# Performance work log

Hardware: AMD Instinct MI355X
Metric: run time of the kernel (lower is better)

## Reference

```python
import jax, jax.numpy as jnp
import numpy as np

D, H, E, K, S = 1024, 2048, 8, 2, 1  # dim, expert hidden, n_experts, top_k, n_shared
B, L = 4, 2048


def setup_inputs() -> dict:
    key = jax.random.key(0)
    ks = jax.random.split(key, 9)
    std = 0.02
    return {
        "x": jax.random.normal(ks[0], (B, L, D), dtype=jnp.float32),
        "router_w": jax.random.normal(ks[1], (E, D), dtype=jnp.float32) * std,
        "experts_bias": jnp.zeros((E,), dtype=jnp.float32),  # aux-free LB bias buffer
        "w1": jax.random.normal(ks[2], (E, D, H), dtype=jnp.float32) * std,
        "w3": jax.random.normal(ks[3], (E, D, H), dtype=jnp.float32) * std,
        "w2": jax.random.normal(ks[4], (E, H, D), dtype=jnp.float32) * std,
        "sw1": jax.random.normal(ks[5], (S, D, H), dtype=jnp.float32) * std,
        "sw3": jax.random.normal(ks[6], (S, D, H), dtype=jnp.float32) * std,
        "sw2": jax.random.normal(ks[7], (S, H, D), dtype=jnp.float32) * std,
    }


def reference(x, router_w, experts_bias, w1, w3, w2, sw1, sw3, sw2):
    b, l, d = x.shape
    xf = x.reshape(-1, d)  # [T, D], T = b*l

    # shared experts (SwiGLU FFN), summed over S
    sg = jnp.einsum("td,sdh->tsh", xf, sw1)
    su = jnp.einsum("td,sdh->tsh", xf, sw3)
    shared_out = jnp.einsum("tsh,shd->td", jax.nn.silu(sg) * su, sw2)

    # router + aux-free load-balancing bias
    logits = xf @ router_w.T + experts_bias  # [T, E]
    rw, sel = jax.lax.top_k(logits, K)       # [T, K]
    rw = jax.nn.softmax(rw.astype(jnp.float32), axis=-1).astype(x.dtype)

    # combine weights scattered to [T, E]; equals torch one_hot dispatch+index_add
    cw = (jax.nn.one_hot(sel, E, dtype=x.dtype) * rw[..., None]).sum(axis=1)

    # all-expert SwiGLU, weighted-combined (identical math: unselected weight = 0)
    g = jnp.einsum("td,edh->teh", xf, w1)
    u = jnp.einsum("td,edh->teh", xf, w3)
    eo = jax.nn.silu(g) * u  # [T, E, H]
    moe_out = jnp.einsum("te,teh,ehd->td", cw, eo, w2)

    return (moe_out + shared_out).reshape(b, l, d)
```

## Files before the change

### kernel.cpp

```cpp
#include <hip/hip_runtime.h>
#include <stdint.h>

#define T_TOK 8192
#define DIMV  1024
#define HIDV  2048
#define NE    8
#define CAP   8192
#define ASSIGN_TOT 24576

typedef __attribute__((ext_vector_type(8))) short          bf16x8;
typedef __attribute__((ext_vector_type(8))) unsigned short u16x8;
typedef __attribute__((ext_vector_type(4))) float          floatx4;

__device__ __forceinline__ unsigned short f2bf(float f) {
    union { float f; unsigned int i; } v; v.f = f;
    unsigned int i = v.i;
    return (unsigned short)((i + 0x7FFFu + ((i >> 16) & 1u)) >> 16);
}

__device__ __forceinline__ void gll16(const void* g, void* l) {
    __builtin_amdgcn_global_load_lds((const __attribute__((address_space(1))) void*)g,
                                     (__attribute__((address_space(3))) void*)l,
                                     16, 0, 0);
}

__global__ __launch_bounds__(256) void router_kernel(
    const float* __restrict__ x,
    const float* __restrict__ rwp,
    const float* __restrict__ biasp,
    unsigned short* __restrict__ xb,
    int* __restrict__ cnt, int* __restrict__ tlist, float* __restrict__ wlist)
{
    const int t    = blockIdx.x * 4 + (threadIdx.x >> 6);
    const int lane = threadIdx.x & 63;
    const float* xr = x + (size_t)t * DIMV + lane * 16;
    float xf[16];
#pragma unroll
    for (int q = 0; q < 4; q++) {
        float4 v = *(const float4*)(xr + q * 4);
        xf[q*4+0] = v.x; xf[q*4+1] = v.y; xf[q*4+2] = v.z; xf[q*4+3] = v.w;
    }
    {
        u16x8 o0, o1;
#pragma unroll
        for (int j = 0; j < 8; j++) { o0[j] = f2bf(xf[j]); o1[j] = f2bf(xf[8 + j]); }
        unsigned short* xo = xb + (size_t)t * DIMV + lane * 16;
        *(u16x8*)xo = o0;
        *(u16x8*)(xo + 8) = o1;
    }
    float acc[NE];
#pragma unroll
    for (int e = 0; e < NE; e++) {
        const float* wr = rwp + (size_t)e * DIMV + lane * 16;
        float s = 0.f;
#pragma unroll
        for (int q = 0; q < 4; q++) {
            float4 v = *(const float4*)(wr + q * 4);
            s += xf[q*4+0]*v.x + xf[q*4+1]*v.y + xf[q*4+2]*v.z + xf[q*4+3]*v.w;
        }
        acc[e] = s;
    }
#pragma unroll
    for (int e = 0; e < NE; e++)
#pragma unroll
        for (int off = 32; off; off >>= 1) acc[e] += __shfl_xor(acc[e], off, 64);

    if (lane == 0) {
        float lg[NE];
#pragma unroll
        for (int e = 0; e < NE; e++) lg[e] = acc[e] + biasp[e];
        int e0 = 0;
#pragma unroll
        for (int e = 1; e < NE; e++) if (lg[e] > lg[e0]) e0 = e;
        int e1 = (e0 == 0) ? 1 : 0;
#pragma unroll
        for (int e = 0; e < NE; e++) if (e != e0 && lg[e] > lg[e1]) e1 = e;
        float z  = __expf(lg[e1] - lg[e0]);
        float p0 = 1.f / (1.f + z);
        float p1 = z  / (1.f + z);
        int s0 = atomicAdd(cnt + e0, 1);
        tlist[e0 * CAP + s0] = t; wlist[e0 * CAP + s0] = p0;
        int s1 = atomicAdd(cnt + e1, 1);
        tlist[e1 * CAP + s1] = t; wlist[e1 * CAP + s1] = p1;
    }
}

__global__ void offsets_kernel(const int* __restrict__ cnt, int* __restrict__ goff)
{
    if (threadIdx.x == 0 && blockIdx.x == 0) {
        int s = 0;
        for (int e = 0; e < NE; e++) { goff[e] = s; s += cnt[e]; }
        goff[NE] = 16384;
    }
}

template<int R, int C>
__device__ __forceinline__ void ctrans_body(
    const float* __restrict__ src, unsigned short* __restrict__ dstp,
    unsigned short (*tile)[66])
{
    const int c0 = blockIdx.x * 64, r0 = blockIdx.y * 64;
    const int tid = threadIdx.x;
    const int lr = tid >> 4;
    const int lc = (tid & 15) * 4;
#pragma unroll
    for (int i = 0; i < 4; i++) {
        int r = lr + 16 * i;
        float4 v = *(const float4*)(src + (size_t)(r0 + r) * C + (c0 + lc));
        ushort4 o; o.x = f2bf(v.x); o.y = f2bf(v.y); o.z = f2bf(v.z); o.w = f2bf(v.w);
        *(ushort4*)&tile[r][lc] = o;
    }
    __syncthreads();
    const int oc  = tid >> 3;
    const int orr = (tid & 7) * 8;
#pragma unroll
    for (int i = 0; i < 2; i++) {
        int c = oc + 32 * i;
        u16x8 tmp;
#pragma unroll
        for (int j = 0; j < 8; j++) tmp[j] = tile[orr + j][c];
        *(u16x8*)(dstp + (size_t)(c0 + c) * R + (r0 + orr)) = tmp;
    }
}

__global__ __launch_bounds__(256) void ctransA_kernel(
    const float* __restrict__ w1, const float* __restrict__ w3,
    const float* __restrict__ sw1, const float* __restrict__ sw3,
    unsigned short* __restrict__ w1t, unsigned short* __restrict__ w3t,
    unsigned short* __restrict__ sw1t, unsigned short* __restrict__ sw3t)
{
    __shared__ unsigned short tile[64][66];
    const int z = blockIdx.z;
    const float* src; unsigned short* dstp;
    if (z < 8)       { src = w1  + (size_t)z * DIMV * HIDV;      dstp = w1t + (size_t)z * DIMV * HIDV; }
    else if (z < 16) { src = w3  + (size_t)(z - 8) * DIMV * HIDV; dstp = w3t + (size_t)(z - 8) * DIMV * HIDV; }
    else if (z == 16){ src = sw1; dstp = sw1t; }
    else             { src = sw3; dstp = sw3t; }
    ctrans_body<DIMV, HIDV>(src, dstp, tile);
}

__global__ __launch_bounds__(256) void ctransB_kernel(
    const float* __restrict__ w2, const float* __restrict__ sw2,
    unsigned short* __restrict__ w2t, unsigned short* __restrict__ sw2t)
{
    __shared__ unsigned short tile[64][66];
    const int z = blockIdx.z;
    const float* src; unsigned short* dstp;
    if (z < 8) { src = w2 + (size_t)z * HIDV * DIMV; dstp = w2t + (size_t)z * HIDV * DIMV; }
    else       { src = sw2; dstp = sw2t; }
    ctrans_body<HIDV, DIMV>(src, dstp, tile);
}

__global__ __launch_bounds__(256, 2) void up_gemm(
    const unsigned short* __restrict__ x,
    const unsigned short* __restrict__ w1t,
    const unsigned short* __restrict__ w3t,
    const unsigned short* __restrict__ sw1t,
    const unsigned short* __restrict__ sw3t,
    const int* __restrict__ cnt, const int* __restrict__ goff,
    const int* __restrict__ tlist,
    unsigned short* __restrict__ hbuf)
{
    const int g = blockIdx.z;
    int n_rows, row_off;
    const unsigned short *B1p, *B3p;
    if (g < NE) {
        n_rows = cnt[g]; row_off = goff[g];
        B1p = w1t + (size_t)g * HIDV * DIMV;
        B3p = w3t + (size_t)g * HIDV * DIMV;
    } else {
        n_rows = T_TOK; row_off = 16384;
        B1p = sw1t; B3p = sw3t;
    }
    const int m0 = blockIdx.y * 128;
    if (m0 >= n_rows) return;
    const int n0 = blockIdx.x * 64;

    __shared__ __align__(16) unsigned short Al[128 * 32];
    __shared__ __align__(16) unsigned short B1l[64 * 32];
    __shared__ __align__(16) unsigned short B3l[64 * 32];

    const int tid  = threadIdx.x;
    const int lane = tid & 63;
    const int wave = tid >> 6;
    const int r0   = tid >> 2;
    const int ck   = (tid & 3) ^ ((r0 >> 1) & 3);

    int tokA, tokB;
    if (g < NE) {
        int ra = m0 + r0, rb = m0 + 64 + r0;
        tokA = (ra < n_rows) ? tlist[g * CAP + ra] : 0;
        tokB = (rb < n_rows) ? tlist[g * CAP + rb] : 0;
    } else { tokA = m0 + r0; tokB = m0 + 64 + r0; }

    const unsigned short* gA0 = x + (size_t)tokA * DIMV + ck * 8;
    const unsigned short* gA1 = x + (size_t)tokB * DIMV + ck * 8;
    const unsigned short* gB1 = B1p + (size_t)(n0 + r0) * DIMV + ck * 8;
    const unsigned short* gB3 = B3p + (size_t)(n0 + r0) * DIMV + ck * 8;

    char* AlB0 = (char*)Al  + wave * 1024;
    char* AlB1 = (char*)Al  + 4096 + wave * 1024;
    char* B1B  = (char*)B1l + wave * 1024;
    char* B3B  = (char*)B3l + wave * 1024;

    const int wm = wave & 1, wn = wave >> 1;
    const int m16 = lane & 15, quad = lane >> 4;
    const int sw  = (m16 >> 1) & 3;

    floatx4 accg[4][2] = {};
    floatx4 accu[4][2] = {};

    const unsigned short* Afp  = Al  + (wm * 64 + m16) * 32 + (quad ^ sw) * 8;
    const unsigned short* B1fp = B1l + (wn * 32 + m16) * 32 + (quad ^ sw) * 8;
    const unsigned short* B3fp = B3l + (wn * 32 + m16) * 32 + (quad ^ sw) * 8;

    for (int k0 = 0; k0 < DIMV; k0 += 32) {
        __syncthreads();
        gll16(gA0 + k0, AlB0);
        gll16(gA1 + k0, AlB1);
        gll16(gB1 + k0, B1B);
        gll16(gB3 + k0, B3B);
        __syncthreads();
        bf16x8 af[4], b1f[2], b3f[2];
#pragma unroll
        for (int i = 0; i < 4; i++) af[i] = *(const bf16x8*)(Afp + i * 16 * 32);
#pragma unroll
        for (int j = 0; j < 2; j++) {
            b1f[j] = *(const bf16x8*)(B1fp + j * 16 * 32);
            b3f[j] = *(const bf16x8*)(B3fp + j * 16 * 32);
        }
#pragma unroll
        for (int i = 0; i < 4; i++)
#pragma unroll
            for (int j = 0; j < 2; j++) {
                accg[i][j] = __builtin_amdgcn_mfma_f32_16x16x32_bf16(af[i], b1f[j], accg[i][j], 0, 0, 0);
                accu[i][j] = __builtin_amdgcn_mfma_f32_16x16x32_bf16(af[i], b3f[j], accu[i][j], 0, 0, 0);
            }
    }

#pragma unroll
    for (int i = 0; i < 4; i++) {
#pragma unroll
        for (int ii = 0; ii < 4; ii++) {
            int r = m0 + wm * 64 + i * 16 + quad * 4 + ii;
            if (r < n_rows) {
#pragma unroll
                for (int j = 0; j < 2; j++) {
                    int col = n0 + wn * 32 + j * 16 + m16;
                    float gv = accg[i][j][ii], uv = accu[i][j][ii];
                    float s  = gv / (1.0f + __expf(-gv));
                    hbuf[(size_t)(row_off + r) * HIDV + col] = f2bf(s * uv);
                }
            }
        }
    }
}

__global__ __launch_bounds__(256, 2) void down_gemm(
    const unsigned short* __restrict__ hbuf,
    const unsigned short* __restrict__ w2t,
    const unsigned short* __restrict__ sw2t,
    const int* __restrict__ cnt, const int* __restrict__ goff,
    const int* __restrict__ tlist, const float* __restrict__ wlist,
    float* __restrict__ outp, int gbase)
{
    const int g = gbase + blockIdx.z;
    int n_rows, row_off;
    const unsigned short* Bp;
    if (g < NE) {
        n_rows = cnt[g]; row_off = goff[g];
        Bp = w2t + (size_t)g * DIMV * HIDV;
    } else {
        n_rows = T_TOK; row_off = 16384;
        Bp = sw2t;
    }
    const int m0 = blockIdx.y * 128;
    if (m0 >= n_rows) return;
    const int n0 = blockIdx.x * 64;

    __shared__ __align__(16) unsigned short Al[128 * 32];
    __shared__ __align__(16) unsigned short Bl[64 * 32];

    const int tid  = threadIdx.x;
    const int lane = tid & 63;
    const int wave = tid >> 6;
    const int r0   = tid >> 2;
    const int ck   = (tid & 3) ^ ((r0 >> 1) & 3);

    const unsigned short* gA0 = hbuf + (size_t)(row_off + m0 + r0) * HIDV + ck * 8;
    const unsigned short* gA1 = hbuf + (size_t)(row_off + m0 + 64 + r0) * HIDV + ck * 8;
    const unsigned short* gB  = Bp + (size_t)(n0 + r0) * HIDV + ck * 8;

    char* AlB0 = (char*)Al + wave * 1024;
    char* AlB1 = (char*)Al + 4096 + wave * 1024;
    char* BB   = (char*)Bl + wave * 1024;

    const int wm = wave & 1, wn = wave >> 1;
    const int m16 = lane & 15, quad = lane >> 4;
    const int sw  = (m16 >> 1) & 3;

    floatx4 acc[4][2] = {};

    const unsigned short* Afp = Al + (wm * 64 + m16) * 32 + (quad ^ sw) * 8;
    const unsigned short* Bfp = Bl + (wn * 32 + m16) * 32 + (quad ^ sw) * 8;

    for (int k0 = 0; k0 < HIDV; k0 += 32) {
        __syncthreads();
        gll16(gA0 + k0, AlB0);
        gll16(gA1 + k0, AlB1);
        gll16(gB  + k0, BB);
        __syncthreads();
        bf16x8 af[4], bf[2];
#pragma unroll
        for (int i = 0; i < 4; i++) af[i] = *(const bf16x8*)(Afp + i * 16 * 32);
#pragma unroll
        for (int j = 0; j < 2; j++) bf[j] = *(const bf16x8*)(Bfp + j * 16 * 32);
#pragma unroll
        for (int i = 0; i < 4; i++)
#pragma unroll
            for (int j = 0; j < 2; j++)
                acc[i][j] = __builtin_amdgcn_mfma_f32_16x16x32_bf16(af[i], bf[j], acc[i][j], 0, 0, 0);
    }

#pragma unroll
    for (int i = 0; i < 4; i++) {
#pragma unroll
        for (int ii = 0; ii < 4; ii++) {
            int r = m0 + wm * 64 + i * 16 + quad * 4 + ii;
            if (r < n_rows) {
                int tok; float wgt;
                if (g < NE) { tok = tlist[g * CAP + r]; wgt = wlist[g * CAP + r]; }
                else        { tok = r;                  wgt = 1.0f; }
#pragma unroll
                for (int j = 0; j < 2; j++) {
                    int col = n0 + wn * 32 + j * 16 + m16;
                    float v = acc[i][j][ii] * wgt;
                    if (g < NE) atomicAdd(outp + (size_t)tok * DIMV + col, v);
                    else        outp[(size_t)tok * DIMV + col] = v;
                }
            }
        }
    }
}

extern "C" void kernel_launch(void* const* d_in, const int* in_sizes, int n_in,
                              void* d_out, int out_size, void* d_ws, size_t ws_size,
                              hipStream_t stream)
{
    (void)in_sizes; (void)n_in; (void)out_size; (void)ws_size;
    const float* x    = (const float*)d_in[0];
    const float* rw   = (const float*)d_in[1];
    const float* bias = (const float*)d_in[2];
    const float* w1   = (const float*)d_in[3];
    const float* w3   = (const float*)d_in[4];
    const float* w2   = (const float*)d_in[5];
    const float* sw1  = (const float*)d_in[6];
    const float* sw3  = (const float*)d_in[7];
    const float* sw2  = (const float*)d_in[8];
    float* outp = (float*)d_out;

    char* p = (char*)d_ws;
    auto alloc = [&](size_t b) { char* r = p; p += (b + 255) & ~(size_t)255; return r; };
    int*   cnt   = (int*)  alloc(64);
    int*   goffp = (int*)  alloc(64);
    int*   tlist = (int*)  alloc((size_t)NE * CAP * 4);
    float* wlist = (float*)alloc((size_t)NE * CAP * 4);
    unsigned short* xb   = (unsigned short*)alloc((size_t)T_TOK * DIMV * 2);
    unsigned short* hbuf = (unsigned short*)alloc((size_t)ASSIGN_TOT * HIDV * 2);
    unsigned short* w1t  = (unsigned short*)alloc((size_t)NE * HIDV * DIMV * 2);
    unsigned short* w3t  = (unsigned short*)alloc((size_t)NE * HIDV * DIMV * 2);
    unsigned short* w2t  = (unsigned short*)alloc((size_t)NE * DIMV * HIDV * 2);
    unsigned short* sw1t = (unsigned short*)alloc((size_t)HIDV * DIMV * 2);
    unsigned short* sw3t = (unsigned short*)alloc((size_t)HIDV * DIMV * 2);
    unsigned short* sw2t = (unsigned short*)alloc((size_t)DIMV * HIDV * 2);

    hipMemsetAsync(cnt, 0, 64, stream);

    dim3 blk(256);
    router_kernel<<<dim3(T_TOK/4), blk, 0, stream>>>(x, rw, bias, xb, cnt, tlist, wlist);
    ctransA_kernel<<<dim3(HIDV/64, DIMV/64, 18), blk, 0, stream>>>(w1, w3, sw1, sw3,
                                                                   w1t, w3t, sw1t, sw3t);
    ctransB_kernel<<<dim3(DIMV/64, HIDV/64, 9),  blk, 0, stream>>>(w2, sw2, w2t, sw2t);
    offsets_kernel<<<dim3(1), dim3(64), 0, stream>>>(cnt, goffp);

    up_gemm<<<dim3(HIDV/64, 64, 9), blk, 0, stream>>>(xb, w1t, w3t, sw1t, sw3t,
                                                      cnt, goffp, tlist, hbuf);
    down_gemm<<<dim3(DIMV/64, 64, 1), blk, 0, stream>>>(hbuf, w2t, sw2t, cnt, goffp,
                                                        tlist, wlist, outp, 8);
    down_gemm<<<dim3(DIMV/64, 64, 8), blk, 0, stream>>>(hbuf, w2t, sw2t, cnt, goffp,
                                                        tlist, wlist, outp, 0);
}
```

Measured before the change: 901.2 us.

## Replace atomic scatter in down GEMM with bf16 staging buffer and gather-combine kernel

The down projection no longer does fp32 atomicAdds into the output. It writes unweighted per-assignment rows in bf16 to a staging buffer that reuses the w1t workspace, and a new combine kernel gathers each token's two routed rows plus its shared row and applies the routing weights. The router now records per-token positions and weights, and the offsets kernel is dropped in favour of inline prefix sums over cnt. The two weight-transpose kernels are merged into one launch, and the down GEMM N tile widens from 64 to 128. This removes atomic contention and extra launches, at the cost of an extra bf16 round trip and an additional kernel.

```diff
diff --git a/kernel.cpp b/kernel.cpp
--- a/kernel.cpp
+++ b/kernel.cpp
@@ -6,6 +6,7 @@
 #define HIDV  2048
 #define NE    8
 #define CAP   8192
+#define ROUTED 16384
 #define ASSIGN_TOT 24576
 
 typedef __attribute__((ext_vector_type(8))) short          bf16x8;
@@ -16,6 +17,9 @@
     union { float f; unsigned int i; } v; v.f = f;
     unsigned int i = v.i;
     return (unsigned short)((i + 0x7FFFu + ((i >> 16) & 1u)) >> 16);
+}
+__device__ __forceinline__ float bf2f(unsigned short u) {
+    union { unsigned int i; float f; } v; v.i = ((unsigned int)u) << 16; return v.f;
 }
 
 __device__ __forceinline__ void gll16(const void* g, void* l) {
@@ -29,7 +33,8 @@
     const float* __restrict__ rwp,
     const float* __restrict__ biasp,
     unsigned short* __restrict__ xb,
-    int* __restrict__ cnt, int* __restrict__ tlist, float* __restrict__ wlist)
+    int* __restrict__ cnt, int* __restrict__ tlist,
+    int* __restrict__ pos, float* __restrict__ pw)
 {
     const int t    = blockIdx.x * 4 + (threadIdx.x >> 6);
     const int lane = threadIdx.x & 63;
@@ -79,18 +84,13 @@
         float p0 = 1.f / (1.f + z);
         float p1 = z  / (1.f + z);
         int s0 = atomicAdd(cnt + e0, 1);
-        tlist[e0 * CAP + s0] = t; wlist[e0 * CAP + s0] = p0;
+        tlist[e0 * CAP + s0] = t;
         int s1 = atomicAdd(cnt + e1, 1);
-        tlist[e1 * CAP + s1] = t; wlist[e1 * CAP + s1] = p1;
-    }
-}
-
-__global__ void offsets_kernel(const int* __restrict__ cnt, int* __restrict__ goff)
-{
-    if (threadIdx.x == 0 && blockIdx.x == 0) {
-        int s = 0;
-        for (int e = 0; e < NE; e++) { goff[e] = s; s += cnt[e]; }
-        goff[NE] = 16384;
+        tlist[e1 * CAP + s1] = t;
+        pos[2 * t + 0] = e0 * CAP + s0;
+        pos[2 * t + 1] = e1 * CAP + s1;
+        pw[2 * t + 0] = p0;
+        pw[2 * t + 1] = p1;
     }
 }
 
@@ -123,32 +123,31 @@
     }
 }
 
-__global__ __launch_bounds__(256) void ctransA_kernel(
+__global__ __launch_bounds__(256) void ctrans_all(
     const float* __restrict__ w1, const float* __restrict__ w3,
     const float* __restrict__ sw1, const float* __restrict__ sw3,
+    const float* __restrict__ w2, const float* __restrict__ sw2,
     unsigned short* __restrict__ w1t, unsigned short* __restrict__ w3t,
-    unsigned short* __restrict__ sw1t, unsigned short* __restrict__ sw3t)
+    unsigned short* __restrict__ sw1t, unsigned short* __restrict__ sw3t,
+    unsigned short* __restrict__ w2t, unsigned short* __restrict__ sw2t)
 {
     __shared__ unsigned short tile[64][66];
     const int z = blockIdx.z;
-    const float* src; unsigned short* dstp;
-    if (z < 8)       { src = w1  + (size_t)z * DIMV * HIDV;      dstp = w1t + (size_t)z * DIMV * HIDV; }
-    else if (z < 16) { src = w3  + (size_t)(z - 8) * DIMV * HIDV; dstp = w3t + (size_t)(z - 8) * DIMV * HIDV; }
-    else if (z == 16){ src = sw1; dstp = sw1t; }
-    else             { src = sw3; dstp = sw3t; }
-    ctrans_body<DIMV, HIDV>(src, dstp, tile);
-}
-
-__global__ __launch_bounds__(256) void ctransB_kernel(
-    const float* __restrict__ w2, const float* __restrict__ sw2,
-    unsigned short* __restrict__ w2t, unsigned short* __restrict__ sw2t)
-{
-    __shared__ unsigned short tile[64][66];
-    const int z = blockIdx.z;
-    const float* src; unsigned short* dstp;
-    if (z < 8) { src = w2 + (size_t)z * HIDV * DIMV; dstp = w2t + (size_t)z * HIDV * DIMV; }
-    else       { src = sw2; dstp = sw2t; }
-    ctrans_body<HIDV, DIMV>(src, dstp, tile);
+    if (z < 18) {
+        if (blockIdx.y >= DIMV / 64) return;
+        const float* src; unsigned short* dstp;
+        if (z < 8)        { src = w1 + (size_t)z * DIMV * HIDV;       dstp = w1t + (size_t)z * DIMV * HIDV; }
+        else if (z < 16)  { src = w3 + (size_t)(z - 8) * DIMV * HIDV; dstp = w3t + (size_t)(z - 8) * DIMV * HIDV; }
+        else if (z == 16) { src = sw1; dstp = sw1t; }
+        else              { src = sw3; dstp = sw3t; }
+        ctrans_body<DIMV, HIDV>(src, dstp, tile);
+    } else {
+        if (blockIdx.x >= DIMV / 64) return;
+        const float* src; unsigned short* dstp;
+        if (z < 26) { src = w2 + (size_t)(z - 18) * HIDV * DIMV; dstp = w2t + (size_t)(z - 18) * HIDV * DIMV; }
+        else        { src = sw2; dstp = sw2t; }
+        ctrans_body<HIDV, DIMV>(src, dstp, tile);
+    }
 }
 
 __global__ __launch_bounds__(256, 2) void up_gemm(
@@ -157,19 +156,20 @@
     const unsigned short* __restrict__ w3t,
     const unsigned short* __restrict__ sw1t,
     const unsigned short* __restrict__ sw3t,
-    const int* __restrict__ cnt, const int* __restrict__ goff,
-    const int* __restrict__ tlist,
+    const int* __restrict__ cnt, const int* __restrict__ tlist,
     unsigned short* __restrict__ hbuf)
 {
     const int g = blockIdx.z;
     int n_rows, row_off;
     const unsigned short *B1p, *B3p;
     if (g < NE) {
-        n_rows = cnt[g]; row_off = goff[g];
+        row_off = 0;
+        for (int e = 0; e < g; e++) row_off += cnt[e];
+        n_rows = cnt[g];
         B1p = w1t + (size_t)g * HIDV * DIMV;
         B3p = w3t + (size_t)g * HIDV * DIMV;
     } else {
-        n_rows = T_TOK; row_off = 16384;
+        n_rows = T_TOK; row_off = ROUTED;
         B1p = sw1t; B3p = sw3t;
     }
     const int m0 = blockIdx.y * 128;
@@ -260,26 +260,27 @@
     const unsigned short* __restrict__ hbuf,
     const unsigned short* __restrict__ w2t,
     const unsigned short* __restrict__ sw2t,
-    const int* __restrict__ cnt, const int* __restrict__ goff,
-    const int* __restrict__ tlist, const float* __restrict__ wlist,
-    float* __restrict__ outp, int gbase)
-{
-    const int g = gbase + blockIdx.z;
+    const int* __restrict__ cnt,
+    unsigned short* __restrict__ dbuf)
+{
+    const int g = blockIdx.z;
     int n_rows, row_off;
     const unsigned short* Bp;
     if (g < NE) {
-        n_rows = cnt[g]; row_off = goff[g];
+        row_off = 0;
+        for (int e = 0; e < g; e++) row_off += cnt[e];
+        n_rows = cnt[g];
         Bp = w2t + (size_t)g * DIMV * HIDV;
     } else {
-        n_rows = T_TOK; row_off = 16384;
+        n_rows = T_TOK; row_off = ROUTED;
         Bp = sw2t;
     }
     const int m0 = blockIdx.y * 128;
     if (m0 >= n_rows) return;
-    const int n0 = blockIdx.x * 64;
+    const int n0 = blockIdx.x * 128;
 
     __shared__ __align__(16) unsigned short Al[128 * 32];
-    __shared__ __align__(16) unsigned short Bl[64 * 32];
+    __shared__ __align__(16) unsigned short Bl[128 * 32];
 
     const int tid  = threadIdx.x;
     const int lane = tid & 63;
@@ -288,37 +289,40 @@
     const int ck   = (tid & 3) ^ ((r0 >> 1) & 3);
 
     const unsigned short* gA0 = hbuf + (size_t)(row_off + m0 + r0) * HIDV + ck * 8;
-    const unsigned short* gA1 = hbuf + (size_t)(row_off + m0 + 64 + r0) * HIDV + ck * 8;
-    const unsigned short* gB  = Bp + (size_t)(n0 + r0) * HIDV + ck * 8;
+    const unsigned short* gA1 = gA0 + (size_t)64 * HIDV;
+    const unsigned short* gB0 = Bp + (size_t)(n0 + r0) * HIDV + ck * 8;
+    const unsigned short* gB1 = gB0 + (size_t)64 * HIDV;
 
     char* AlB0 = (char*)Al + wave * 1024;
     char* AlB1 = (char*)Al + 4096 + wave * 1024;
-    char* BB   = (char*)Bl + wave * 1024;
+    char* BB0  = (char*)Bl + wave * 1024;
+    char* BB1  = (char*)Bl + 4096 + wave * 1024;
 
     const int wm = wave & 1, wn = wave >> 1;
     const int m16 = lane & 15, quad = lane >> 4;
     const int sw  = (m16 >> 1) & 3;
 
-    floatx4 acc[4][2] = {};
+    floatx4 acc[4][4] = {};
 
     const unsigned short* Afp = Al + (wm * 64 + m16) * 32 + (quad ^ sw) * 8;
-    const unsigned short* Bfp = Bl + (wn * 32 + m16) * 32 + (quad ^ sw) * 8;
+    const unsigned short* Bfp = Bl + (wn * 64 + m16) * 32 + (quad ^ sw) * 8;
 
     for (int k0 = 0; k0 < HIDV; k0 += 32) {
         __syncthreads();
         gll16(gA0 + k0, AlB0);
         gll16(gA1 + k0, AlB1);
-        gll16(gB  + k0, BB);
+        gll16(gB0 + k0, BB0);
+        gll16(gB1 + k0, BB1);
         __syncthreads();
-        bf16x8 af[4], bf[2];
+        bf16x8 af[4], bf[4];
 #pragma unroll
         for (int i = 0; i < 4; i++) af[i] = *(const bf16x8*)(Afp + i * 16 * 32);
 #pragma unroll
-        for (int j = 0; j < 2; j++) bf[j] = *(const bf16x8*)(Bfp + j * 16 * 32);
+        for (int j = 0; j < 4; j++) bf[j] = *(const bf16x8*)(Bfp + j * 16 * 32);
 #pragma unroll
         for (int i = 0; i < 4; i++)
 #pragma unroll
-            for (int j = 0; j < 2; j++)
+            for (int j = 0; j < 4; j++)
                 acc[i][j] = __builtin_amdgcn_mfma_f32_16x16x32_bf16(af[i], bf[j], acc[i][j], 0, 0, 0);
     }
 
@@ -328,19 +332,45 @@
         for (int ii = 0; ii < 4; ii++) {
             int r = m0 + wm * 64 + i * 16 + quad * 4 + ii;
             if (r < n_rows) {
-                int tok; float wgt;
-                if (g < NE) { tok = tlist[g * CAP + r]; wgt = wlist[g * CAP + r]; }
-                else        { tok = r;                  wgt = 1.0f; }
-#pragma unroll
-                for (int j = 0; j < 2; j++) {
-                    int col = n0 + wn * 32 + j * 16 + m16;
-                    float v = acc[i][j][ii] * wgt;
-                    if (g < NE) atomicAdd(outp + (size_t)tok * DIMV + col, v);
-                    else        outp[(size_t)tok * DIMV + col] = v;
+                unsigned short* drow = dbuf + (size_t)(row_off + r) * DIMV;
+#pragma unroll
+                for (int j = 0; j < 4; j++) {
+                    int col = n0 + wn * 64 + j * 16 + m16;
+                    drow[col] = f2bf(acc[i][j][ii]);
                 }
             }
         }
     }
+}
+
+__global__ __launch_bounds__(256) void combine_kernel(
+    const unsigned short* __restrict__ dbuf,
+    const int* __restrict__ cnt, const int* __restrict__ pos,
+    const float* __restrict__ pw, float* __restrict__ outp)
+{
+    const int tid = threadIdx.x;
+    const int t = blockIdx.x * 2 + (tid >> 7);
+    const int c = (tid & 127) * 8;
+    int goff[NE];
+    {
+        int s = 0;
+#pragma unroll
+        for (int e = 0; e < NE; e++) { goff[e] = s; s += cnt[e]; }
+    }
+    const int p0 = pos[2 * t], p1 = pos[2 * t + 1];
+    const float w0 = pw[2 * t], w1 = pw[2 * t + 1];
+    const int r0 = goff[p0 >> 13] + (p0 & (CAP - 1));
+    const int r1 = goff[p1 >> 13] + (p1 & (CAP - 1));
+    const u16x8 v0 = *(const u16x8*)(dbuf + (size_t)r0 * DIMV + c);
+    const u16x8 v1 = *(const u16x8*)(dbuf + (size_t)r1 * DIMV + c);
+    const u16x8 vs = *(const u16x8*)(dbuf + (size_t)(ROUTED + t) * DIMV + c);
+    float o[8];
+#pragma unroll
+    for (int j = 0; j < 8; j++)
+        o[j] = w0 * bf2f(v0[j]) + w1 * bf2f(v1[j]) + bf2f(vs[j]);
+    float* op = outp + (size_t)t * DIMV + c;
+    *(float4*)op       = make_float4(o[0], o[1], o[2], o[3]);
+    *(float4*)(op + 4) = make_float4(o[4], o[5], o[6], o[7]);
 }
 
 extern "C" void kernel_launch(void* const* d_in, const int* in_sizes, int n_in,
@@ -362,9 +392,9 @@
     char* p = (char*)d_ws;
     auto alloc = [&](size_t b) { char* r = p; p += (b + 255) & ~(size_t)255; return r; };
     int*   cnt   = (int*)  alloc(64);
-    int*   goffp = (int*)  alloc(64);
     int*   tlist = (int*)  alloc((size_t)NE * CAP * 4);
-    float* wlist = (float*)alloc((size_t)NE * CAP * 4);
+    int*   pos   = (int*)  alloc((size_t)T_TOK * 2 * 4);
+    float* pw    = (float*)alloc((size_t)T_TOK * 2 * 4);
     unsigned short* xb   = (unsigned short*)alloc((size_t)T_TOK * DIMV * 2);
     unsigned short* hbuf = (unsigned short*)alloc((size_t)ASSIGN_TOT * HIDV * 2);
     unsigned short* w1t  = (unsigned short*)alloc((size_t)NE * HIDV * DIMV * 2);
@@ -373,20 +403,16 @@
     unsigned short* sw1t = (unsigned short*)alloc((size_t)HIDV * DIMV * 2);
     unsigned short* sw3t = (unsigned short*)alloc((size_t)HIDV * DIMV * 2);
     unsigned short* sw2t = (unsigned short*)alloc((size_t)DIMV * HIDV * 2);
+    unsigned short* dbuf = w1t;
 
     hipMemsetAsync(cnt, 0, 64, stream);
 
     dim3 blk(256);
-    router_kernel<<<dim3(T_TOK/4), blk, 0, stream>>>(x, rw, bias, xb, cnt, tlist, wlist);
-    ctransA_kernel<<<dim3(HIDV/64, DIMV/64, 18), blk, 0, stream>>>(w1, w3, sw1, sw3,
-                                                                   w1t, w3t, sw1t, sw3t);
-    ctransB_kernel<<<dim3(DIMV/64, HIDV/64, 9),  blk, 0, stream>>>(w2, sw2, w2t, sw2t);
-    offsets_kernel<<<dim3(1), dim3(64), 0, stream>>>(cnt, goffp);
-
+    router_kernel<<<dim3(T_TOK/4), blk, 0, stream>>>(x, rw, bias, xb, cnt, tlist, pos, pw);
+    ctrans_all<<<dim3(HIDV/64, HIDV/64, 27), blk, 0, stream>>>(w1, w3, sw1, sw3, w2, sw2,
+                                                               w1t, w3t, sw1t, sw3t, w2t, sw2t);
     up_gemm<<<dim3(HIDV/64, 64, 9), blk, 0, stream>>>(xb, w1t, w3t, sw1t, sw3t,
-                                                      cnt, goffp, tlist, hbuf);
-    down_gemm<<<dim3(DIMV/64, 64, 1), blk, 0, stream>>>(hbuf, w2t, sw2t, cnt, goffp,
-                                                        tlist, wlist, outp, 8);
-    down_gemm<<<dim3(DIMV/64, 64, 8), blk, 0, stream>>>(hbuf, w2t, sw2t, cnt, goffp,
-                                                        tlist, wlist, outp, 0);
-}
+                                                      cnt, tlist, hbuf);
+    down_gemm<<<dim3(DIMV/128, 64, 9), blk, 0, stream>>>(hbuf, w2t, sw2t, cnt, dbuf);
+    combine_kernel<<<dim3(T_TOK/2), blk, 0, stream>>>(dbuf, cnt, pos, pw, outp);
+}
```

Result: faster. 851.8 us (-5.5%).
